# Kernel tuning notes

Hardware: AMD Instinct MI355X
Metric: run time of the kernel (lower is better)

The kernel has to match this reference:

```python
import jax, jax.numpy as jnp
import numpy as np
import math

HIDDEN = 2048
N_HEADS = 16
HEAD_DIM = HIDDEN // N_HEADS
ROPE_BASE = 10000.0


def setup_inputs() -> dict:
    key = jax.random.key(0)
    ks = jax.random.split(key, 5)
    B, S = 2, 2048
    hidden_states = jax.random.normal(ks[0], (B, S, HIDDEN), dtype=jnp.float32)
    # additive causal mask (bsz, 1, q_len, kv_len)
    causal = jnp.tril(jnp.ones((S, S), dtype=bool))
    attention_mask = jnp.where(causal, 0.0, jnp.finfo(jnp.float32).min)[None, None].astype(jnp.float32)
    attention_mask = jnp.broadcast_to(attention_mask, (B, 1, S, S))
    position_ids = jnp.broadcast_to(jnp.arange(S, dtype=jnp.int32)[None], (B, S))
    scale = 1.0 / math.sqrt(HIDDEN)
    Wq = jax.random.normal(ks[1], (HIDDEN, HIDDEN), dtype=jnp.float32) * scale
    Wk = jax.random.normal(ks[2], (HIDDEN, HIDDEN), dtype=jnp.float32) * scale
    Wv = jax.random.normal(ks[3], (HIDDEN, HIDDEN), dtype=jnp.float32) * scale
    Wo = jax.random.normal(ks[4], (HIDDEN, HIDDEN), dtype=jnp.float32) * scale
    return {"hidden_states": hidden_states, "attention_mask": attention_mask,
            "position_ids": position_ids, "Wq": Wq, "Wk": Wk, "Wv": Wv, "Wo": Wo}


def _rotate_half(x):
    x1, x2 = jnp.split(x, 2, axis=-1)
    return jnp.concatenate([-x2, x1], axis=-1)


def _rope_cos_sin(position_ids, head_dim, dtype):
    inv_freq = 1.0 / (ROPE_BASE ** (jnp.arange(0, head_dim, 2, dtype=jnp.float32) / head_dim))
    freqs = position_ids.astype(jnp.float32)[..., None] * inv_freq  # [B, S, hd/2]
    emb = jnp.concatenate([freqs, freqs], axis=-1)                  # [B, S, hd]
    # unsqueeze head dim -> [B, 1, S, hd]
    return jnp.cos(emb)[:, None].astype(dtype), jnp.sin(emb)[:, None].astype(dtype)


def reference(hidden_states, attention_mask, position_ids, Wq, Wk, Wv, Wo):
    B, S, _ = hidden_states.shape
    H, D = N_HEADS, HEAD_DIM
    # projections (nn.Linear: x @ W.T); split heads -> [B, H, S, D]
    def proj(W):
        return jnp.einsum('bsh,oh->bso', hidden_states, W).reshape(B, S, H, D).transpose(0, 2, 1, 3)
    q, k, v = proj(Wq), proj(Wk), proj(Wv)
    cos, sin = _rope_cos_sin(position_ids, D, hidden_states.dtype)
    q = q * cos + _rotate_half(q) * sin
    k = k * cos + _rotate_half(k) * sin
    scores = jnp.einsum('bhqd,bhkd->bhqk', q, k) / math.sqrt(D)
    scores = scores + attention_mask
    probs = jax.nn.softmax(scores.astype(jnp.float32), axis=-1).astype(q.dtype)
    attn = jnp.einsum('bhqk,bhkd->bhqd', probs, v)
    attn = attn.transpose(0, 2, 1, 3).reshape(B, S, H * D)
    return jnp.einsum('bso,ho->bsh', attn, Wo)
```

## Files before the change

kernel.cpp:

```cpp
#include <hip/hip_runtime.h>
#include <cstdint>

typedef unsigned short u16t;
typedef float v4f __attribute__((ext_vector_type(4)));
typedef short v8s __attribute__((ext_vector_type(8)));

#define HIDDEN 2048
#define NHEAD 16
#define HDIM 128
#define SEQ 2048
#define BATCH 2
#define MROWS (BATCH * SEQ)

__device__ __forceinline__ float bf2f(u16t u) {
  return __builtin_bit_cast(float, (uint32_t)((uint32_t)u << 16));
}
__device__ __forceinline__ u16t f2bf(float f) {
  uint32_t u = __builtin_bit_cast(uint32_t, f);
  u += 0x7FFFu + ((u >> 16) & 1u);
  return (u16t)(u >> 16);
}
__device__ __forceinline__ ushort4 f2bf4(float4 v) {
  ushort4 r;
  r.x = f2bf(v.x); r.y = f2bf(v.y); r.z = f2bf(v.z); r.w = f2bf(v.w);
  return r;
}

__device__ __forceinline__ void gld_lds16(const u16t* g, u16t* l) {
  __builtin_amdgcn_global_load_lds(
      (const __attribute__((address_space(1))) uint32_t*)g,
      (__attribute__((address_space(3))) uint32_t*)l, 16, 0, 0);
}

__global__ __launch_bounds__(256) void cvt_bf16(const float* __restrict__ src,
                                                u16t* __restrict__ dst, int n8) {
  int i = blockIdx.x * 256 + threadIdx.x;
  if (i < n8) {
    float4 a = ((const float4*)src)[2 * i];
    float4 b = ((const float4*)src)[2 * i + 1];
    union { ushort4 h[2]; uint4 u; } pk;
    pk.h[0] = f2bf4(a);
    pk.h[1] = f2bf4(b);
    ((uint4*)dst)[i] = pk.u;
  }
}

__global__ __launch_bounds__(256) void cvt_bf16_w4(
    const float* __restrict__ s0, const float* __restrict__ s1,
    const float* __restrict__ s2, const float* __restrict__ s3,
    u16t* __restrict__ d0, u16t* __restrict__ d1,
    u16t* __restrict__ d2, u16t* __restrict__ d3) {
  int i = blockIdx.x * 256 + threadIdx.x;
  int sel = i >> 19;
  int j = i & 0x7FFFF;
  const float* src = (sel == 0) ? s0 : (sel == 1) ? s1 : (sel == 2) ? s2 : s3;
  u16t* dst = (sel == 0) ? d0 : (sel == 1) ? d1 : (sel == 2) ? d2 : d3;
  float4 a = ((const float4*)src)[2 * j];
  float4 b = ((const float4*)src)[2 * j + 1];
  union { ushort4 h[2]; uint4 u; } pk;
  pk.h[0] = f2bf4(a);
  pk.h[1] = f2bf4(b);
  ((uint4*)dst)[j] = pk.u;
}

template <int MODE>
__global__ __launch_bounds__(512) void gemm_fused(const u16t* __restrict__ A,
                                                  const u16t* __restrict__ B,
                                                  u16t* __restrict__ qo,
                                                  u16t* __restrict__ ko,
                                                  u16t* __restrict__ vto,
                                                  float* __restrict__ fo) {
  __shared__ u16t lds[49152];

  const int NX = (MODE == 0) ? 24 : 8;
  const int CPX = (MODE == 0) ? 48 : 16;
  const int id = blockIdx.x;
  const int swz = (id & 7) * CPX + (id >> 3);
  const int tx = swz % NX;
  const int ty = swz / NX;
  const int n0 = tx * 256;
  const int m0 = ty * 256;

  const int t = threadIdx.x;
  const int lane = t & 63;
  const int w = t >> 6;
  const int wm = w >> 2;
  const int wn = w & 3;
  const int l15 = lane & 15;
  const int quad = lane >> 4;

  const int srow = t >> 2;
  const int sc8 = ((t & 3) ^ ((t >> 3) & 3)) * 8;
  const u16t* Ag = A + (size_t)(m0 + srow) * HIDDEN + sc8;
  const u16t* Bg = B + (size_t)(n0 + srow) * HIDDEN + sc8;

  const int pcol = (quad ^ ((l15 >> 1) & 3)) * 8;

  v4f acc[8][4];
#pragma unroll
  for (int i = 0; i < 8; ++i)
#pragma unroll
    for (int j = 0; j < 4; ++j) acc[i][j] = (v4f){0.f, 0.f, 0.f, 0.f};

  const int KT = HIDDEN / 32;

#pragma unroll
  for (int tt = 0; tt < 2; ++tt) {
    const int kb = tt * 32;
    gld_lds16(Ag + kb, &lds[tt * 8192 + t * 8]);
    gld_lds16(Ag + kb + 128 * HIDDEN, &lds[tt * 8192 + 4096 + t * 8]);
    gld_lds16(Bg + kb, &lds[24576 + tt * 8192 + t * 8]);
    gld_lds16(Bg + kb + 128 * HIDDEN, &lds[24576 + tt * 8192 + 4096 + t * 8]);
  }
  asm volatile("s_waitcnt vmcnt(4)" ::: "memory");
  __builtin_amdgcn_s_barrier();

  int b = 0;
  for (int kt = 0; kt < KT; ++kt) {
    const int kb2 = kt * 32 + 64;
    const int b2 = (b >= 1) ? b - 1 : 2;
    const u16t* Asb = &lds[b * 8192];
    const u16t* Bsb = &lds[24576 + b * 8192];
    const bool pre = (kt + 2 < KT);

    v8s bfr[4];
#pragma unroll
    for (int j = 0; j < 4; ++j)
      bfr[j] = *(const v8s*)&Bsb[(wn * 64 + j * 16 + l15) * 32 + pcol];
    v8s af[4];
#pragma unroll
    for (int i = 0; i < 4; ++i)
      af[i] = *(const v8s*)&Asb[(wm * 128 + i * 16 + l15) * 32 + pcol];
    if (pre) {
      gld_lds16(Ag + kb2, &lds[b2 * 8192 + t * 8]);
      gld_lds16(Bg + kb2, &lds[24576 + b2 * 8192 + t * 8]);
    }
    __builtin_amdgcn_s_barrier();
    asm volatile("s_waitcnt lgkmcnt(0)" ::: "memory");
    __builtin_amdgcn_s_setprio(1);
#pragma unroll
    for (int i = 0; i < 4; ++i)
#pragma unroll
      for (int j = 0; j < 4; ++j)
        acc[i][j] = __builtin_amdgcn_mfma_f32_16x16x32_bf16(af[i], bfr[j], acc[i][j], 0, 0, 0);
    __builtin_amdgcn_s_setprio(0);
    __builtin_amdgcn_s_barrier();

#pragma unroll
    for (int i = 0; i < 4; ++i)
      af[i] = *(const v8s*)&Asb[(wm * 128 + 64 + i * 16 + l15) * 32 + pcol];
    if (pre) {
      gld_lds16(Ag + kb2 + 128 * HIDDEN, &lds[b2 * 8192 + 4096 + t * 8]);
      gld_lds16(Bg + kb2 + 128 * HIDDEN, &lds[24576 + b2 * 8192 + 4096 + t * 8]);
    }
    __builtin_amdgcn_s_barrier();
    asm volatile("s_waitcnt lgkmcnt(0)" ::: "memory");
    __builtin_amdgcn_s_setprio(1);
#pragma unroll
    for (int i = 0; i < 4; ++i)
#pragma unroll
      for (int j = 0; j < 4; ++j)
        acc[4 + i][j] = __builtin_amdgcn_mfma_f32_16x16x32_bf16(af[i], bfr[j], acc[4 + i][j], 0, 0, 0);
    __builtin_amdgcn_s_setprio(0);
    if (pre) {
      asm volatile("s_waitcnt vmcnt(4)" ::: "memory");
    } else if (kt + 1 < KT) {
      asm volatile("s_waitcnt vmcnt(0)" ::: "memory");
    }
    __builtin_amdgcn_s_barrier();
    b = (b == 2) ? 0 : b + 1;
  }

  if (MODE == 1) {
#pragma unroll
    for (int i = 0; i < 8; ++i) {
#pragma unroll
      for (int j = 0; j < 4; ++j) {
        int col = n0 + wn * 64 + j * 16 + l15;
#pragma unroll
        for (int r = 0; r < 4; ++r) {
          int row = m0 + wm * 128 + i * 16 + quad * 4 + r;
          fo[(size_t)row * HIDDEN + col] = acc[i][j][r];
        }
      }
    }
  } else if (tx < 16) {
    u16t* dst = (tx < 8) ? qo : ko;
    const int cb = n0 & 2047;
#pragma unroll
    for (int i = 0; i < 8; ++i) {
#pragma unroll
      for (int j = 0; j < 4; ++j) {
        int col = cb + wn * 64 + j * 16 + l15;
#pragma unroll
        for (int r = 0; r < 4; ++r) {
          int row = m0 + wm * 128 + i * 16 + quad * 4 + r;
          dst[(size_t)row * HIDDEN + col] = f2bf(acc[i][j][r]);
        }
      }
    }
  } else {
    const int nv0 = n0 - 4096;
    u16t* Ct = (u16t*)lds;
#pragma unroll
    for (int h = 0; h < 2; ++h) {
      __syncthreads();
      if ((wn >> 1) == h) {
#pragma unroll
        for (int i = 0; i < 8; ++i)
#pragma unroll
          for (int j = 0; j < 4; ++j)
#pragma unroll
            for (int r = 0; r < 4; ++r)
              Ct[((wn & 1) * 64 + j * 16 + l15) * 264 +
                 wm * 128 + i * 16 + quad * 4 + r] = f2bf(acc[i][j][r]);
      }
      __syncthreads();
#pragma unroll
      for (int it = 0; it < 8; ++it) {
        int idx = t + it * 512;
        int nl = idx >> 5;
        int mc = idx & 31;
        *(uint4*)&vto[(size_t)(nv0 + h * 128 + nl) * MROWS + m0 + mc * 8] =
            *(const uint4*)&Ct[nl * 264 + mc * 8];
      }
    }
  }
}

template <int OUT_F32>
__global__ __launch_bounds__(256) void gemm_a16(const u16t* __restrict__ A,
                                                const void* __restrict__ Bp,
                                                void* __restrict__ Cp) {
  __shared__ u16t As[128 * 32];
  __shared__ u16t Bs[128 * 32];

  const int n0 = blockIdx.x * 128;
  const int m0 = blockIdx.y * 128;
  const int t = threadIdx.x;
  const int lane = t & 63;
  const int w = t >> 6;
  const int wm = w & 1;
  const int wn = w >> 1;
  const int l15 = lane & 15;
  const int quad = lane >> 4;

  v4f acc[4][4];
#pragma unroll
  for (int i = 0; i < 4; ++i)
#pragma unroll
    for (int j = 0; j < 4; ++j) acc[i][j] = (v4f){0.f, 0.f, 0.f, 0.f};

  for (int kb = 0; kb < HIDDEN; kb += 32) {
#pragma unroll
    for (int j = 0; j < 2; ++j) {
      int idx = t + j * 256;
      int row = idx >> 2;
      int ch = (idx & 3) * 8;
      gld_lds16(&A[(size_t)(m0 + row) * HIDDEN + kb + ch], &As[idx * 8]);
    }
    {
      const float* B = (const float*)Bp;
#pragma unroll
      for (int j = 0; j < 4; ++j) {
        int idx = t + j * 256;
        int row = idx >> 3;
        int c4 = (idx & 7) * 4;
        float4 bv = *(const float4*)&B[(size_t)(n0 + row) * HIDDEN + kb + c4];
        *(ushort4*)&Bs[row * 32 + c4] = f2bf4(bv);
      }
    }
    __syncthreads();

    v8s af[4], bf[4];
#pragma unroll
    for (int mt = 0; mt < 4; ++mt)
      af[mt] = *(const v8s*)&As[(wm * 64 + mt * 16 + l15) * 32 + quad * 8];
#pragma unroll
    for (int nt = 0; nt < 4; ++nt)
      bf[nt] = *(const v8s*)&Bs[(wn * 64 + nt * 16 + l15) * 32 + quad * 8];

#pragma unroll
    for (int mt = 0; mt < 4; ++mt)
#pragma unroll
      for (int nt = 0; nt < 4; ++nt)
        acc[mt][nt] = __builtin_amdgcn_mfma_f32_16x16x32_bf16(af[mt], bf[nt], acc[mt][nt], 0, 0, 0);
    __syncthreads();
  }

#pragma unroll
  for (int mt = 0; mt < 4; ++mt) {
#pragma unroll
    for (int nt = 0; nt < 4; ++nt) {
      int col = n0 + wn * 64 + nt * 16 + l15;
#pragma unroll
      for (int r = 0; r < 4; ++r) {
        int row = m0 + wm * 64 + mt * 16 + quad * 4 + r;
        if (OUT_F32)
          ((float*)Cp)[(size_t)row * HIDDEN + col] = acc[mt][nt][r];
        else
          ((u16t*)Cp)[(size_t)row * HIDDEN + col] = f2bf(acc[mt][nt][r]);
      }
    }
  }
}

__global__ __launch_bounds__(256) void gemm_vt_f32(const u16t* __restrict__ A,
                                                   const void* __restrict__ Bp,
                                                   u16t* __restrict__ VtOut) {
  __shared__ u16t As[128 * 32];
  __shared__ u16t Bs[128 * 32];
  __shared__ u16t Ct[128 * 136];

  const int n0 = blockIdx.x * 128;
  const int m0 = blockIdx.y * 128;
  const int t = threadIdx.x;
  const int lane = t & 63;
  const int w = t >> 6;
  const int wm = w & 1;
  const int wn = w >> 1;
  const int l15 = lane & 15;
  const int quad = lane >> 4;

  v4f acc[4][4];
#pragma unroll
  for (int i = 0; i < 4; ++i)
#pragma unroll
    for (int j = 0; j < 4; ++j) acc[i][j] = (v4f){0.f, 0.f, 0.f, 0.f};

  for (int kb = 0; kb < HIDDEN; kb += 32) {
#pragma unroll
    for (int j = 0; j < 2; ++j) {
      int idx = t + j * 256;
      int row = idx >> 2;
      int ch = (idx & 3) * 8;
      gld_lds16(&A[(size_t)(m0 + row) * HIDDEN + kb + ch], &As[idx * 8]);
    }
    {
      const float* B = (const float*)Bp;
#pragma unroll
      for (int j = 0; j < 4; ++j) {
        int idx = t + j * 256;
        int row = idx >> 3;
        int c4 = (idx & 7) * 4;
        float4 bv = *(const float4*)&B[(size_t)(n0 + row) * HIDDEN + kb + c4];
        *(ushort4*)&Bs[row * 32 + c4] = f2bf4(bv);
      }
    }
    __syncthreads();

    v8s af[4], bf[4];
#pragma unroll
    for (int mt = 0; mt < 4; ++mt)
      af[mt] = *(const v8s*)&As[(wm * 64 + mt * 16 + l15) * 32 + quad * 8];
#pragma unroll
    for (int nt = 0; nt < 4; ++nt)
      bf[nt] = *(const v8s*)&Bs[(wn * 64 + nt * 16 + l15) * 32 + quad * 8];

#pragma unroll
    for (int mt = 0; mt < 4; ++mt)
#pragma unroll
      for (int nt = 0; nt < 4; ++nt)
        acc[mt][nt] = __builtin_amdgcn_mfma_f32_16x16x32_bf16(af[mt], bf[nt], acc[mt][nt], 0, 0, 0);
    __syncthreads();
  }

#pragma unroll
  for (int mt = 0; mt < 4; ++mt)
#pragma unroll
    for (int nt = 0; nt < 4; ++nt)
#pragma unroll
      for (int r = 0; r < 4; ++r)
        Ct[(wn * 64 + nt * 16 + l15) * 136 + (wm * 64 + mt * 16 + quad * 4 + r)] =
            f2bf(acc[mt][nt][r]);
  __syncthreads();

#pragma unroll
  for (int j = 0; j < 8; ++j) {
    int idx = t + j * 256;
    int nl = idx >> 4;
    int mc = idx & 15;
    *(uint4*)&VtOut[(size_t)(n0 + nl) * MROWS + m0 + mc * 8] =
        *(const uint4*)&Ct[nl * 136 + mc * 8];
  }
}

__global__ __launch_bounds__(256) void rope_k(u16t* __restrict__ q, u16t* __restrict__ k) {
  int idx = blockIdx.x * 256 + threadIdx.x;
  int i = idx & 63;
  int h = (idx >> 6) & (NHEAD - 1);
  int m = idx >> 10;
  int s = m & (SEQ - 1);
  float inv = __expf(-(float)i * 0.14391156831212787f);
  float th = (float)s * inv;
  float sn, cs;
  __sincosf(th, &sn, &cs);
  size_t base = (size_t)m * HIDDEN + h * HDIM + i;
  {
    float a = bf2f(q[base]), b = bf2f(q[base + 64]);
    q[base] = f2bf(a * cs - b * sn);
    q[base + 64] = f2bf(b * cs + a * sn);
  }
  {
    float a = bf2f(k[base]), b = bf2f(k[base + 64]);
    k[base] = f2bf(a * cs - b * sn);
    k[base + 64] = f2bf(b * cs + a * sn);
  }
}

__global__ __launch_bounds__(512) void flash2(const u16t* __restrict__ Q,
                                              const u16t* __restrict__ K,
                                              const u16t* __restrict__ Vt,
                                              u16t* __restrict__ O) {
  __shared__ u16t smem[40960];
  u16t* Ps = smem + 32768;

  const int a = blockIdx.x;
  const int bh = blockIdx.y;
  const int b = bh >> 4;
  const int h = bh & 15;
  const size_t rowb = (size_t)b * SEQ;
  const u16t* vtg = Vt + (size_t)h * HDIM * MROWS + (size_t)b * SEQ;

  const int t = threadIdx.x;
  const int lane = t & 63;
  const int w = t >> 6;
  const int l15 = lane & 15;
  const int quad = lane >> 4;
  const int l7 = l15 & 7;
  const float C2 = 0.12751743f;
  const float NEG = -3.0e38f;

  const int krow = t >> 4;
  const int kch = (t & 15) * 8;
  const int vrow = t >> 3;
  const int vch = (t & 7) * 8;
  const int kx = kch ^ ((krow & 7) * 8);
  const int vx = vch ^ ((vrow & 7) * 8);
  const u16t* Kgb = &K[(rowb + krow) * HIDDEN + h * HDIM + kch];
  const u16t* Vgb = vtg + (size_t)vrow * MROWS + vch;

  for (int half = 0; half < 2; ++half) {
    const int qt = half ? (15 - a) : a;
    const int q0 = qt * 128;
    const int nsteps = 2 * (qt + 1);

    uint4 ck0 = *(const uint4*)Kgb;
    uint4 ck1 = *(const uint4*)(Kgb + 32 * HIDDEN);
    uint4 cv0 = *(const uint4*)Vgb;
    uint4 cv1 = *(const uint4*)(Vgb + (size_t)64 * MROWS);

#pragma unroll
    for (int j = 0; j < 4; ++j) {
      int idx = t + j * 512;
      int row = idx >> 4;
      int ch = (idx & 15) * 8;
      *(uint4*)&smem[row * 136 + ch] =
          *(const uint4*)&Q[(rowb + q0 + row) * HIDDEN + h * HDIM + ch];
    }
    __syncthreads();
    v8s qf[4];
#pragma unroll
    for (int ks = 0; ks < 4; ++ks)
      qf[ks] = *(const v8s*)&smem[(w * 16 + l15) * 136 + ks * 32 + quad * 8];
    __syncthreads();

    float mi[4], li[4];
    v4f o[8];
#pragma unroll
    for (int r = 0; r < 4; ++r) { mi[r] = NEG; li[r] = 0.f; }
#pragma unroll
    for (int nt = 0; nt < 8; ++nt) o[nt] = (v4f){0.f, 0.f, 0.f, 0.f};

    for (int kt = 0; kt < nsteps; ++kt) {
      u16t* Kb = smem + (kt & 1) * 16384;
      u16t* Vb = Kb + 8192;
      *(uint4*)&Kb[krow * 128 + kx] = ck0;
      *(uint4*)&Kb[(krow + 32) * 128 + kx] = ck1;
      *(uint4*)&Vb[vrow * 64 + vx] = cv0;
      *(uint4*)&Vb[(vrow + 64) * 64 + vx] = cv1;
      if (kt + 1 < nsteps) {
        const int kv1 = (kt + 1) * 64;
        const u16t* kg = Kgb + (size_t)kv1 * HIDDEN;
        ck0 = *(const uint4*)kg;
        ck1 = *(const uint4*)(kg + 32 * HIDDEN);
        const u16t* vg = Vgb + kv1;
        cv0 = *(const uint4*)vg;
        cv1 = *(const uint4*)(vg + (size_t)64 * MROWS);
      }
      __syncthreads();

      const int kv0 = kt * 64;
      v4f sc[4];
#pragma unroll
      for (int nt = 0; nt < 4; ++nt) {
        sc[nt] = (v4f){0.f, 0.f, 0.f, 0.f};
#pragma unroll
        for (int ks = 0; ks < 4; ++ks) {
          v8s kf = *(const v8s*)&Kb[(nt * 16 + l15) * 128 +
                                    ((ks * 32 + quad * 8) ^ (l7 * 8))];
          sc[nt] = __builtin_amdgcn_mfma_f32_16x16x32_bf16(qf[ks], kf, sc[nt], 0, 0, 0);
        }
      }

      const bool mm = (kv0 + 64 > q0);
#pragma unroll
      for (int r = 0; r < 4; ++r) {
        float sv[4];
#pragma unroll
        for (int nt = 0; nt < 4; ++nt) sv[nt] = sc[nt][r];
        if (mm) {
          int row_g = q0 + w * 16 + quad * 4 + r;
#pragma unroll
          for (int nt = 0; nt < 4; ++nt)
            if (kv0 + nt * 16 + l15 > row_g) sv[nt] = NEG;
        }
        float rm = fmaxf(fmaxf(sv[0], sv[1]), fmaxf(sv[2], sv[3]));
#pragma unroll
        for (int off = 1; off < 16; off <<= 1) rm = fmaxf(rm, __shfl_xor(rm, off));
        float mn = fmaxf(mi[r], rm);
        float alpha = exp2f((mi[r] - mn) * C2);
        float ps = 0.f;
        u16t pb[4];
#pragma unroll
        for (int nt = 0; nt < 4; ++nt) {
          float p = exp2f((sv[nt] - mn) * C2);
          ps += p;
          pb[nt] = f2bf(p);
        }
#pragma unroll
        for (int off = 1; off < 16; off <<= 1) ps += __shfl_xor(ps, off);
        li[r] = li[r] * alpha + ps;
        mi[r] = mn;
#pragma unroll
        for (int nt = 0; nt < 8; ++nt) o[nt][r] *= alpha;
        int rowp = w * 16 + quad * 4 + r;
        int psw = (rowp & 7) * 8;
#pragma unroll
        for (int nt = 0; nt < 4; ++nt)
          Ps[rowp * 64 + ((nt * 16 + l15) ^ psw)] = pb[nt];
      }

#pragma unroll
      for (int ks = 0; ks < 2; ++ks) {
        v8s pf = *(const v8s*)&Ps[(w * 16 + l15) * 64 +
                                  ((ks * 32 + quad * 8) ^ (l7 * 8))];
#pragma unroll
        for (int nt = 0; nt < 8; ++nt) {
          v8s vf = *(const v8s*)&Vb[(nt * 16 + l15) * 64 +
                                    ((ks * 32 + quad * 8) ^ (l7 * 8))];
          o[nt] = __builtin_amdgcn_mfma_f32_16x16x32_bf16(pf, vf, o[nt], 0, 0, 0);
        }
      }
    }

#pragma unroll
    for (int r = 0; r < 4; ++r) {
      float inv = 1.0f / li[r];
      size_t row = rowb + q0 + w * 16 + quad * 4 + r;
#pragma unroll
      for (int nt = 0; nt < 8; ++nt)
        O[row * HIDDEN + h * HDIM + nt * 16 + l15] = f2bf(o[nt][r] * inv);
    }
    __syncthreads();
  }
}

extern "C" void kernel_launch(void* const* d_in, const int* in_sizes, int n_in,
                              void* d_out, int out_size, void* d_ws, size_t ws_size,
                              hipStream_t stream) {
  const float* X = (const float*)d_in[0];
  const float* Wq = (const float*)d_in[3];
  const float* Wk = (const float*)d_in[4];
  const float* Wv = (const float*)d_in[5];
  const float* Wo = (const float*)d_in[6];
  float* out = (float*)d_out;

  char* wsb = (char*)d_ws;
  const size_t MB = 1024 * 1024;
  u16t* xb = (u16t*)(wsb + 0 * MB);
  u16t* q = (u16t*)(wsb + 16 * MB);
  u16t* k = (u16t*)(wsb + 32 * MB);
  u16t* vt = (u16t*)(wsb + 48 * MB);
  u16t* a = xb;

  dim3 blk(256);
  dim3 fg(8, BATCH * NHEAD);
  const int XN8 = MROWS * HIDDEN / 8;
  const int WN8 = HIDDEN * HIDDEN / 8;

  cvt_bf16<<<(XN8 + 255) / 256, blk, 0, stream>>>(X, xb, XN8);

  if (ws_size >= 96 * MB) {
    u16t* wqb = (u16t*)(wsb + 64 * MB);
    u16t* wkb = (u16t*)(wsb + 72 * MB);
    u16t* wvb = (u16t*)(wsb + 80 * MB);
    u16t* wob = (u16t*)(wsb + 88 * MB);
    cvt_bf16_w4<<<(4 * WN8) / 256, blk, 0, stream>>>(Wq, Wk, Wv, Wo, wqb, wkb, wvb, wob);

    gemm_fused<0><<<dim3(384), dim3(512), 0, stream>>>(xb, wqb, q, k, vt, nullptr);
    rope_k<<<(MROWS * NHEAD * 64) / 256, blk, 0, stream>>>(q, k);
    flash2<<<fg, dim3(512), 0, stream>>>(q, k, vt, a);
    gemm_fused<1><<<dim3(128), dim3(512), 0, stream>>>(a, wob, nullptr, nullptr, nullptr, out);
  } else {
    dim3 gg(HIDDEN / 128, MROWS / 128);
    gemm_a16<0><<<gg, blk, 0, stream>>>(xb, Wq, q);
    gemm_a16<0><<<gg, blk, 0, stream>>>(xb, Wk, k);
    gemm_vt_f32<<<gg, blk, 0, stream>>>(xb, Wv, vt);
    rope_k<<<(MROWS * NHEAD * 64) / 256, blk, 0, stream>>>(q, k);
    flash2<<<fg, dim3(512), 0, stream>>>(q, k, vt, a);
    gemm_a16<1><<<gg, blk, 0, stream>>>(a, Wo, out);
  }
}
```

Baseline: 440.3 us.

## Deepen GEMM pipeline to four stages, narrow output GEMM tile, lazy softmax rescale

```diff
diff --git a/kernel.cpp b/kernel.cpp
--- a/kernel.cpp
+++ b/kernel.cpp
@@ -64,21 +64,27 @@
 }
 
 template <int MODE>
-__global__ __launch_bounds__(512) void gemm_fused(const u16t* __restrict__ A,
-                                                  const u16t* __restrict__ B,
-                                                  u16t* __restrict__ qo,
-                                                  u16t* __restrict__ ko,
-                                                  u16t* __restrict__ vto,
-                                                  float* __restrict__ fo) {
-  __shared__ u16t lds[49152];
-
-  const int NX = (MODE == 0) ? 24 : 8;
-  const int CPX = (MODE == 0) ? 48 : 16;
+__global__ __launch_bounds__(512) void gemm_pipe(const u16t* __restrict__ A,
+                                                 const u16t* __restrict__ B,
+                                                 u16t* __restrict__ qo,
+                                                 u16t* __restrict__ ko,
+                                                 u16t* __restrict__ vto,
+                                                 float* __restrict__ fo) {
+  constexpr int BN = (MODE == 0) ? 256 : 128;
+  constexpr int NX = (MODE == 0) ? 24 : 16;
+  constexpr int CPX = (MODE == 0) ? 48 : 32;
+  constexpr int NF = BN / 64;
+  constexpr int BBUF = BN * 32;
+
+  __shared__ u16t lds[32768 + 4 * BBUF];
+  u16t* Alds = lds;
+  u16t* Blds = lds + 32768;
+
   const int id = blockIdx.x;
   const int swz = (id & 7) * CPX + (id >> 3);
   const int tx = swz % NX;
   const int ty = swz / NX;
-  const int n0 = tx * 256;
+  const int n0 = tx * BN;
   const int m0 = ty * 256;
 
   const int t = threadIdx.x;
@@ -96,44 +102,50 @@
 
   const int pcol = (quad ^ ((l15 >> 1) & 3)) * 8;
 
-  v4f acc[8][4];
+  v4f acc[8][NF];
 #pragma unroll
   for (int i = 0; i < 8; ++i)
 #pragma unroll
-    for (int j = 0; j < 4; ++j) acc[i][j] = (v4f){0.f, 0.f, 0.f, 0.f};
+    for (int j = 0; j < NF; ++j) acc[i][j] = (v4f){0.f, 0.f, 0.f, 0.f};
 
   const int KT = HIDDEN / 32;
 
 #pragma unroll
-  for (int tt = 0; tt < 2; ++tt) {
+  for (int tt = 0; tt < 3; ++tt) {
     const int kb = tt * 32;
-    gld_lds16(Ag + kb, &lds[tt * 8192 + t * 8]);
-    gld_lds16(Ag + kb + 128 * HIDDEN, &lds[tt * 8192 + 4096 + t * 8]);
-    gld_lds16(Bg + kb, &lds[24576 + tt * 8192 + t * 8]);
-    gld_lds16(Bg + kb + 128 * HIDDEN, &lds[24576 + tt * 8192 + 4096 + t * 8]);
-  }
-  asm volatile("s_waitcnt vmcnt(4)" ::: "memory");
+    gld_lds16(Ag + kb, &Alds[tt * 8192 + t * 8]);
+    gld_lds16(Ag + kb + 128 * HIDDEN, &Alds[tt * 8192 + 4096 + t * 8]);
+    gld_lds16(Bg + kb, &Blds[tt * BBUF + t * 8]);
+    if (MODE == 0)
+      gld_lds16(Bg + kb + 128 * HIDDEN, &Blds[tt * BBUF + 4096 + t * 8]);
+  }
+  if (MODE == 0)
+    asm volatile("s_waitcnt vmcnt(8)" ::: "memory");
+  else
+    asm volatile("s_waitcnt vmcnt(6)" ::: "memory");
   __builtin_amdgcn_s_barrier();
 
-  int b = 0;
   for (int kt = 0; kt < KT; ++kt) {
-    const int kb2 = kt * 32 + 64;
-    const int b2 = (b >= 1) ? b - 1 : 2;
-    const u16t* Asb = &lds[b * 8192];
-    const u16t* Bsb = &lds[24576 + b * 8192];
-    const bool pre = (kt + 2 < KT);
-
-    v8s bfr[4];
-#pragma unroll
-    for (int j = 0; j < 4; ++j)
-      bfr[j] = *(const v8s*)&Bsb[(wn * 64 + j * 16 + l15) * 32 + pcol];
+    const int bu = kt & 3;
+    const int b3 = (kt + 3) & 3;
+    const int kb3 = kt * 32 + 96;
+    const u16t* Asb = &Alds[bu * 8192];
+    const u16t* Bsb = &Blds[bu * BBUF];
+    const bool pre = (kt + 3 < KT);
+
+    v8s bfr[NF];
+#pragma unroll
+    for (int j = 0; j < NF; ++j)
+      bfr[j] = *(const v8s*)&Bsb[(wn * (BN / 4) + j * 16 + l15) * 32 + pcol];
     v8s af[4];
 #pragma unroll
     for (int i = 0; i < 4; ++i)
       af[i] = *(const v8s*)&Asb[(wm * 128 + i * 16 + l15) * 32 + pcol];
     if (pre) {
-      gld_lds16(Ag + kb2, &lds[b2 * 8192 + t * 8]);
-      gld_lds16(Bg + kb2, &lds[24576 + b2 * 8192 + t * 8]);
+      gld_lds16(Ag + kb3, &Alds[b3 * 8192 + t * 8]);
+      gld_lds16(Bg + kb3, &Blds[b3 * BBUF + t * 8]);
+      if (MODE == 1)
+        gld_lds16(Ag + kb3 + 128 * HIDDEN, &Alds[b3 * 8192 + 4096 + t * 8]);
     }
     __builtin_amdgcn_s_barrier();
     asm volatile("s_waitcnt lgkmcnt(0)" ::: "memory");
@@ -141,7 +153,7 @@
 #pragma unroll
     for (int i = 0; i < 4; ++i)
 #pragma unroll
-      for (int j = 0; j < 4; ++j)
+      for (int j = 0; j < NF; ++j)
         acc[i][j] = __builtin_amdgcn_mfma_f32_16x16x32_bf16(af[i], bfr[j], acc[i][j], 0, 0, 0);
     __builtin_amdgcn_s_setprio(0);
     __builtin_amdgcn_s_barrier();
@@ -150,8 +162,10 @@
     for (int i = 0; i < 4; ++i)
       af[i] = *(const v8s*)&Asb[(wm * 128 + 64 + i * 16 + l15) * 32 + pcol];
     if (pre) {
-      gld_lds16(Ag + kb2 + 128 * HIDDEN, &lds[b2 * 8192 + 4096 + t * 8]);
-      gld_lds16(Bg + kb2 + 128 * HIDDEN, &lds[24576 + b2 * 8192 + 4096 + t * 8]);
+      if (MODE == 0) {
+        gld_lds16(Ag + kb3 + 128 * HIDDEN, &Alds[b3 * 8192 + 4096 + t * 8]);
+        gld_lds16(Bg + kb3 + 128 * HIDDEN, &Blds[b3 * BBUF + 4096 + t * 8]);
+      }
     }
     __builtin_amdgcn_s_barrier();
     asm volatile("s_waitcnt lgkmcnt(0)" ::: "memory");
@@ -159,24 +173,31 @@
 #pragma unroll
     for (int i = 0; i < 4; ++i)
 #pragma unroll
-      for (int j = 0; j < 4; ++j)
+      for (int j = 0; j < NF; ++j)
         acc[4 + i][j] = __builtin_amdgcn_mfma_f32_16x16x32_bf16(af[i], bfr[j], acc[4 + i][j], 0, 0, 0);
     __builtin_amdgcn_s_setprio(0);
-    if (pre) {
-      asm volatile("s_waitcnt vmcnt(4)" ::: "memory");
+    if (kt + 3 < KT) {
+      if (MODE == 0)
+        asm volatile("s_waitcnt vmcnt(8)" ::: "memory");
+      else
+        asm volatile("s_waitcnt vmcnt(6)" ::: "memory");
+    } else if (kt + 2 < KT) {
+      if (MODE == 0)
+        asm volatile("s_waitcnt vmcnt(4)" ::: "memory");
+      else
+        asm volatile("s_waitcnt vmcnt(3)" ::: "memory");
     } else if (kt + 1 < KT) {
       asm volatile("s_waitcnt vmcnt(0)" ::: "memory");
     }
     __builtin_amdgcn_s_barrier();
-    b = (b == 2) ? 0 : b + 1;
   }
 
   if (MODE == 1) {
 #pragma unroll
     for (int i = 0; i < 8; ++i) {
 #pragma unroll
-      for (int j = 0; j < 4; ++j) {
-        int col = n0 + wn * 64 + j * 16 + l15;
+      for (int j = 0; j < NF; ++j) {
+        int col = n0 + wn * (BN / 4) + j * 16 + l15;
 #pragma unroll
         for (int r = 0; r < 4; ++r) {
           int row = m0 + wm * 128 + i * 16 + quad * 4 + r;
@@ -190,7 +211,7 @@
 #pragma unroll
     for (int i = 0; i < 8; ++i) {
 #pragma unroll
-      for (int j = 0; j < 4; ++j) {
+      for (int j = 0; j < NF; ++j) {
         int col = cb + wn * 64 + j * 16 + l15;
 #pragma unroll
         for (int r = 0; r < 4; ++r) {
@@ -209,7 +230,7 @@
 #pragma unroll
         for (int i = 0; i < 8; ++i)
 #pragma unroll
-          for (int j = 0; j < 4; ++j)
+          for (int j = 0; j < NF; ++j)
 #pragma unroll
             for (int r = 0; r < 4; ++r)
               Ct[((wn & 1) * 64 + j * 16 + l15) * 264 +
@@ -518,22 +539,24 @@
         float rm = fmaxf(fmaxf(sv[0], sv[1]), fmaxf(sv[2], sv[3]));
 #pragma unroll
         for (int off = 1; off < 16; off <<= 1) rm = fmaxf(rm, __shfl_xor(rm, off));
-        float mn = fmaxf(mi[r], rm);
-        float alpha = exp2f((mi[r] - mn) * C2);
+        if (rm > mi[r] + 7.84f) {
+          float alpha = exp2f((mi[r] - rm) * C2);
+          mi[r] = rm;
+          li[r] *= alpha;
+#pragma unroll
+          for (int nt = 0; nt < 8; ++nt) o[nt][r] *= alpha;
+        }
         float ps = 0.f;
         u16t pb[4];
 #pragma unroll
         for (int nt = 0; nt < 4; ++nt) {
-          float p = exp2f((sv[nt] - mn) * C2);
+          float p = exp2f((sv[nt] - mi[r]) * C2);
           ps += p;
           pb[nt] = f2bf(p);
         }
 #pragma unroll
         for (int off = 1; off < 16; off <<= 1) ps += __shfl_xor(ps, off);
-        li[r] = li[r] * alpha + ps;
-        mi[r] = mn;
-#pragma unroll
-        for (int nt = 0; nt < 8; ++nt) o[nt][r] *= alpha;
+        li[r] += ps;
         int rowp = w * 16 + quad * 4 + r;
         int psw = (rowp & 7) * 8;
 #pragma unroll
@@ -598,10 +621,10 @@
     u16t* wob = (u16t*)(wsb + 88 * MB);
     cvt_bf16_w4<<<(4 * WN8) / 256, blk, 0, stream>>>(Wq, Wk, Wv, Wo, wqb, wkb, wvb, wob);
 
-    gemm_fused<0><<<dim3(384), dim3(512), 0, stream>>>(xb, wqb, q, k, vt, nullptr);
+    gemm_pipe<0><<<dim3(384), dim3(512), 0, stream>>>(xb, wqb, q, k, vt, nullptr);
     rope_k<<<(MROWS * NHEAD * 64) / 256, blk, 0, stream>>>(q, k);
     flash2<<<fg, dim3(512), 0, stream>>>(q, k, vt, a);
-    gemm_fused<1><<<dim3(128), dim3(512), 0, stream>>>(a, wob, nullptr, nullptr, nullptr, out);
+    gemm_pipe<1><<<dim3(256), dim3(512), 0, stream>>>(a, wob, nullptr, nullptr, nullptr, out);
   } else {
     dim3 gg(HIDDEN / 128, MROWS / 128);
     gemm_a16<0><<<gg, blk, 0, stream>>>(xb, Wq, q);
```

Result: no change. 433.8 us (-1.5%).

## Restructure GEMM into 8-phase K=64 double-buffered pipeline and lazy softmax rescale

Applied to the files above, without the earlier changes.

```diff
diff --git a/kernel.cpp b/kernel.cpp
--- a/kernel.cpp
+++ b/kernel.cpp
@@ -63,17 +63,33 @@
   ((uint4*)dst)[j] = pk.u;
 }
 
-template <int MODE>
-__global__ __launch_bounds__(512) void gemm_fused(const u16t* __restrict__ A,
-                                                  const u16t* __restrict__ B,
-                                                  u16t* __restrict__ qo,
-                                                  u16t* __restrict__ ko,
-                                                  u16t* __restrict__ vto,
-                                                  float* __restrict__ fo) {
-  __shared__ u16t lds[49152];
-
-  const int NX = (MODE == 0) ? 24 : 8;
-  const int CPX = (MODE == 0) ? 48 : 16;
+#define STG_A(h, kt_, bb)                                                      \
+  do {                                                                         \
+    gld_lds16(A + (size_t)(m0 + (h) * 128 + r0) * HIDDEN + (kt_) * 64 + c0,   \
+              lds + (bb) * 16384 + (h) * 8192 + t * 8);                        \
+    gld_lds16(A + (size_t)(m0 + (h) * 128 + r1) * HIDDEN + (kt_) * 64 + c1,   \
+              lds + (bb) * 16384 + (h) * 8192 + 4096 + t * 8);                 \
+  } while (0)
+
+#define STG_B(h, kt_, bb)                                                      \
+  do {                                                                         \
+    gld_lds16(B + (size_t)(n0 + (h) * 128 + r0) * HIDDEN + (kt_) * 64 + c0,   \
+              lds + 32768 + (bb) * 16384 + (h) * 8192 + t * 8);                \
+    gld_lds16(B + (size_t)(n0 + (h) * 128 + r1) * HIDDEN + (kt_) * 64 + c1,   \
+              lds + 32768 + (bb) * 16384 + (h) * 8192 + 4096 + t * 8);         \
+  } while (0)
+
+template <int EPI>
+__global__ __launch_bounds__(512) void gemm8p(const u16t* __restrict__ A,
+                                              const u16t* __restrict__ B,
+                                              u16t* __restrict__ qo,
+                                              u16t* __restrict__ ko,
+                                              u16t* __restrict__ vto,
+                                              float* __restrict__ fo) {
+  __shared__ u16t lds[65536];
+
+  constexpr int NX = (EPI == 0) ? 24 : 8;
+  constexpr int CPX = (EPI == 0) ? 48 : 16;
   const int id = blockIdx.x;
   const int swz = (id & 7) * CPX + (id >> 3);
   const int tx = swz % NX;
@@ -88,13 +104,15 @@
   const int wn = w & 3;
   const int l15 = lane & 15;
   const int quad = lane >> 4;
-
-  const int srow = t >> 2;
-  const int sc8 = ((t & 3) ^ ((t >> 3) & 3)) * 8;
-  const u16t* Ag = A + (size_t)(m0 + srow) * HIDDEN + sc8;
-  const u16t* Bg = B + (size_t)(n0 + srow) * HIDDEN + sc8;
-
-  const int pcol = (quad ^ ((l15 >> 1) & 3)) * 8;
+  const int l7 = l15 & 7;
+
+  const int r0 = t >> 3;
+  const int c0 = ((t & 7) ^ (r0 & 7)) * 8;
+  const int r1 = (t + 512) >> 3;
+  const int c1 = ((t & 7) ^ (r1 & 7)) * 8;
+
+  const int ca0 = (quad ^ l7) * 8;
+  const int ca1 = ((4 + quad) ^ l7) * 8;
 
   v4f acc[8][4];
 #pragma unroll
@@ -102,76 +120,106 @@
 #pragma unroll
     for (int j = 0; j < 4; ++j) acc[i][j] = (v4f){0.f, 0.f, 0.f, 0.f};
 
-  const int KT = HIDDEN / 32;
-
-#pragma unroll
-  for (int tt = 0; tt < 2; ++tt) {
-    const int kb = tt * 32;
-    gld_lds16(Ag + kb, &lds[tt * 8192 + t * 8]);
-    gld_lds16(Ag + kb + 128 * HIDDEN, &lds[tt * 8192 + 4096 + t * 8]);
-    gld_lds16(Bg + kb, &lds[24576 + tt * 8192 + t * 8]);
-    gld_lds16(Bg + kb + 128 * HIDDEN, &lds[24576 + tt * 8192 + 4096 + t * 8]);
-  }
+  const int KT = HIDDEN / 64;
+
+  STG_A(0, 0, 0); STG_A(1, 0, 0); STG_B(0, 0, 0); STG_B(1, 0, 0);
+  STG_A(0, 1, 1); STG_B(0, 1, 1);
   asm volatile("s_waitcnt vmcnt(4)" ::: "memory");
   __builtin_amdgcn_s_barrier();
 
-  int b = 0;
   for (int kt = 0; kt < KT; ++kt) {
-    const int kb2 = kt * 32 + 64;
-    const int b2 = (b >= 1) ? b - 1 : 2;
-    const u16t* Asb = &lds[b * 8192];
-    const u16t* Bsb = &lds[24576 + b * 8192];
-    const bool pre = (kt + 2 < KT);
-
-    v8s bfr[4];
-#pragma unroll
-    for (int j = 0; j < 4; ++j)
-      bfr[j] = *(const v8s*)&Bsb[(wn * 64 + j * 16 + l15) * 32 + pcol];
-    v8s af[4];
-#pragma unroll
-    for (int i = 0; i < 4; ++i)
-      af[i] = *(const v8s*)&Asb[(wm * 128 + i * 16 + l15) * 32 + pcol];
-    if (pre) {
-      gld_lds16(Ag + kb2, &lds[b2 * 8192 + t * 8]);
-      gld_lds16(Bg + kb2, &lds[24576 + b2 * 8192 + t * 8]);
-    }
+    const int bi = kt & 1;
+    const int bo = bi ^ 1;
+    const u16t* Asb = lds + bi * 16384 + wm * 8192;
+    const u16t* Bsb = lds + 32768 + bi * 16384;
+
+    v8s A0[4], A1[4], Bq0[2], Bq1[2], Br0[2], Br1[2];
+
+#pragma unroll
+    for (int i = 0; i < 4; ++i) {
+      const u16t* p = Asb + (i * 16 + l15) * 64;
+      A0[i] = *(const v8s*)(p + ca0);
+      A1[i] = *(const v8s*)(p + ca1);
+    }
+#pragma unroll
+    for (int j = 0; j < 2; ++j) {
+      const u16t* p = Bsb + (wn * 64 + j * 16 + l15) * 64;
+      Bq0[j] = *(const v8s*)(p + ca0);
+      Bq1[j] = *(const v8s*)(p + ca1);
+    }
+    if (kt + 1 < KT) { STG_A(1, kt + 1, bo); }
     __builtin_amdgcn_s_barrier();
     asm volatile("s_waitcnt lgkmcnt(0)" ::: "memory");
     __builtin_amdgcn_s_setprio(1);
 #pragma unroll
     for (int i = 0; i < 4; ++i)
 #pragma unroll
-      for (int j = 0; j < 4; ++j)
-        acc[i][j] = __builtin_amdgcn_mfma_f32_16x16x32_bf16(af[i], bfr[j], acc[i][j], 0, 0, 0);
+      for (int j = 0; j < 2; ++j) {
+        acc[i][j] = __builtin_amdgcn_mfma_f32_16x16x32_bf16(A0[i], Bq0[j], acc[i][j], 0, 0, 0);
+        acc[i][j] = __builtin_amdgcn_mfma_f32_16x16x32_bf16(A1[i], Bq1[j], acc[i][j], 0, 0, 0);
+      }
     __builtin_amdgcn_s_setprio(0);
     __builtin_amdgcn_s_barrier();
 
 #pragma unroll
-    for (int i = 0; i < 4; ++i)
-      af[i] = *(const v8s*)&Asb[(wm * 128 + 64 + i * 16 + l15) * 32 + pcol];
-    if (pre) {
-      gld_lds16(Ag + kb2 + 128 * HIDDEN, &lds[b2 * 8192 + 4096 + t * 8]);
-      gld_lds16(Bg + kb2 + 128 * HIDDEN, &lds[24576 + b2 * 8192 + 4096 + t * 8]);
-    }
+    for (int j = 0; j < 2; ++j) {
+      const u16t* p = Bsb + (wn * 64 + (2 + j) * 16 + l15) * 64;
+      Br0[j] = *(const v8s*)(p + ca0);
+      Br1[j] = *(const v8s*)(p + ca1);
+    }
+    if (kt + 1 < KT) { STG_B(1, kt + 1, bo); }
     __builtin_amdgcn_s_barrier();
     asm volatile("s_waitcnt lgkmcnt(0)" ::: "memory");
     __builtin_amdgcn_s_setprio(1);
 #pragma unroll
     for (int i = 0; i < 4; ++i)
 #pragma unroll
-      for (int j = 0; j < 4; ++j)
-        acc[4 + i][j] = __builtin_amdgcn_mfma_f32_16x16x32_bf16(af[i], bfr[j], acc[4 + i][j], 0, 0, 0);
+      for (int j = 0; j < 2; ++j) {
+        acc[i][2 + j] = __builtin_amdgcn_mfma_f32_16x16x32_bf16(A0[i], Br0[j], acc[i][2 + j], 0, 0, 0);
+        acc[i][2 + j] = __builtin_amdgcn_mfma_f32_16x16x32_bf16(A1[i], Br1[j], acc[i][2 + j], 0, 0, 0);
+      }
     __builtin_amdgcn_s_setprio(0);
-    if (pre) {
+    __builtin_amdgcn_s_barrier();
+
+#pragma unroll
+    for (int i = 0; i < 4; ++i) {
+      const u16t* p = Asb + ((4 + i) * 16 + l15) * 64;
+      A0[i] = *(const v8s*)(p + ca0);
+      A1[i] = *(const v8s*)(p + ca1);
+    }
+    if (kt + 2 < KT) { STG_B(0, kt + 2, bi); }
+    __builtin_amdgcn_s_barrier();
+    asm volatile("s_waitcnt lgkmcnt(0)" ::: "memory");
+    __builtin_amdgcn_s_setprio(1);
+#pragma unroll
+    for (int i = 0; i < 4; ++i)
+#pragma unroll
+      for (int j = 0; j < 2; ++j) {
+        acc[4 + i][j] = __builtin_amdgcn_mfma_f32_16x16x32_bf16(A0[i], Bq0[j], acc[4 + i][j], 0, 0, 0);
+        acc[4 + i][j] = __builtin_amdgcn_mfma_f32_16x16x32_bf16(A1[i], Bq1[j], acc[4 + i][j], 0, 0, 0);
+      }
+    __builtin_amdgcn_s_setprio(0);
+    __builtin_amdgcn_s_barrier();
+
+    if (kt + 2 < KT) { STG_A(0, kt + 2, bi); }
+    __builtin_amdgcn_s_setprio(1);
+#pragma unroll
+    for (int i = 0; i < 4; ++i)
+#pragma unroll
+      for (int j = 0; j < 2; ++j) {
+        acc[4 + i][2 + j] = __builtin_amdgcn_mfma_f32_16x16x32_bf16(A0[i], Br0[j], acc[4 + i][2 + j], 0, 0, 0);
+        acc[4 + i][2 + j] = __builtin_amdgcn_mfma_f32_16x16x32_bf16(A1[i], Br1[j], acc[4 + i][2 + j], 0, 0, 0);
+      }
+    __builtin_amdgcn_s_setprio(0);
+    if (kt + 2 < KT) {
       asm volatile("s_waitcnt vmcnt(4)" ::: "memory");
-    } else if (kt + 1 < KT) {
+    } else {
       asm volatile("s_waitcnt vmcnt(0)" ::: "memory");
     }
     __builtin_amdgcn_s_barrier();
-    b = (b == 2) ? 0 : b + 1;
-  }
-
-  if (MODE == 1) {
+  }
+
+  if (EPI == 1) {
 #pragma unroll
     for (int i = 0; i < 8; ++i) {
 #pragma unroll
@@ -227,6 +275,8 @@
     }
   }
 }
+#undef STG_A
+#undef STG_B
 
 template <int OUT_F32>
 __global__ __launch_bounds__(256) void gemm_a16(const u16t* __restrict__ A,
@@ -518,22 +568,24 @@
         float rm = fmaxf(fmaxf(sv[0], sv[1]), fmaxf(sv[2], sv[3]));
 #pragma unroll
         for (int off = 1; off < 16; off <<= 1) rm = fmaxf(rm, __shfl_xor(rm, off));
-        float mn = fmaxf(mi[r], rm);
-        float alpha = exp2f((mi[r] - mn) * C2);
+        if (rm > mi[r] + 7.84f) {
+          float alpha = exp2f((mi[r] - rm) * C2);
+          mi[r] = rm;
+          li[r] *= alpha;
+#pragma unroll
+          for (int nt = 0; nt < 8; ++nt) o[nt][r] *= alpha;
+        }
         float ps = 0.f;
         u16t pb[4];
 #pragma unroll
         for (int nt = 0; nt < 4; ++nt) {
-          float p = exp2f((sv[nt] - mn) * C2);
+          float p = exp2f((sv[nt] - mi[r]) * C2);
           ps += p;
           pb[nt] = f2bf(p);
         }
 #pragma unroll
         for (int off = 1; off < 16; off <<= 1) ps += __shfl_xor(ps, off);
-        li[r] = li[r] * alpha + ps;
-        mi[r] = mn;
-#pragma unroll
-        for (int nt = 0; nt < 8; ++nt) o[nt][r] *= alpha;
+        li[r] += ps;
         int rowp = w * 16 + quad * 4 + r;
         int psw = (rowp & 7) * 8;
 #pragma unroll
@@ -598,10 +650,10 @@
     u16t* wob = (u16t*)(wsb + 88 * MB);
     cvt_bf16_w4<<<(4 * WN8) / 256, blk, 0, stream>>>(Wq, Wk, Wv, Wo, wqb, wkb, wvb, wob);
 
-    gemm_fused<0><<<dim3(384), dim3(512), 0, stream>>>(xb, wqb, q, k, vt, nullptr);
+    gemm8p<0><<<dim3(384), dim3(512), 0, stream>>>(xb, wqb, q, k, vt, nullptr);
     rope_k<<<(MROWS * NHEAD * 64) / 256, blk, 0, stream>>>(q, k);
     flash2<<<fg, dim3(512), 0, stream>>>(q, k, vt, a);
-    gemm_fused<1><<<dim3(128), dim3(512), 0, stream>>>(a, wob, nullptr, nullptr, nullptr, out);
+    gemm8p<1><<<dim3(128), dim3(512), 0, stream>>>(a, wob, nullptr, nullptr, nullptr, out);
   } else {
     dim3 gg(HIDDEN / 128, MROWS / 128);
     gemm_a16<0><<<gg, blk, 0, stream>>>(xb, Wq, q);
```

Result: no change. 435.5 us (-1.1%).
